# Optimization experiments

Hardware: AMD Instinct MI355X
Metric: run time of the kernel (lower is better)

The kernel has to match this reference:

```python
import jax, jax.numpy as jnp
import numpy as np

B, T, C, H = 8, 2048, 768, 64  # batch, block_size, n_embd, head_size

def setup_inputs() -> dict:
    key = jax.random.key(0)
    kx, kk, kq, kv = jax.random.split(key, 4)
    x = jax.random.normal(kx, (B, T, C), dtype=jnp.float32)
    Wk = jax.random.normal(kk, (C, H), dtype=jnp.float32) * (C ** -0.5)
    Wq = jax.random.normal(kq, (C, H), dtype=jnp.float32) * (C ** -0.5)
    Wv = jax.random.normal(kv, (C, H), dtype=jnp.float32) * (C ** -0.5)
    return {"x": x, "Wk": Wk, "Wq": Wq, "Wv": Wv}

def reference(x, Wk, Wq, Wv):
    # single causal self-attention head (dropout in eval mode = identity)
    k = jnp.einsum('btc,ch->bth', x, Wk)  # [B,T,H]
    q = jnp.einsum('btc,ch->bth', x, Wq)
    v = jnp.einsum('btc,ch->bth', x, Wv)
    scale = jnp.asarray(k.shape[-1], x.dtype) ** -0.5
    wei = jnp.einsum('bth,bsh->bts', q, k) * scale  # [B,T,T]
    t = x.shape[1]
    causal = jnp.tril(jnp.ones((t, t), dtype=bool))
    wei = jnp.where(causal[None, :, :], wei, jnp.asarray(-jnp.inf, wei.dtype))
    wei = jax.nn.softmax(wei, axis=-1)
    out = jnp.einsum('bts,bsh->bth', wei, v)  # [B,T,H]
    return out
```

## Files before the change

### kernel.cpp

```cpp
#include <hip/hip_runtime.h>
#include <hip/hip_bf16.h>

typedef __attribute__((ext_vector_type(8))) short short8;
typedef __attribute__((ext_vector_type(4))) float f32x4;

#define B_  8
#define T_  2048
#define C_  768
#define H_  64
#define M_  (B_ * T_)

static __device__ __forceinline__ unsigned short f2bf(float f) {
    __hip_bfloat16 h = __float2bfloat16(f);
    return *reinterpret_cast<unsigned short*>(&h);
}

static __device__ __forceinline__ short8 make_frag(const unsigned short* p0, const unsigned short* p1) {
    const ushort4 a = *reinterpret_cast<const ushort4*>(p0);
    const ushort4 b = *reinterpret_cast<const ushort4*>(p1);
    short8 r;
    r[0] = (short)a.x; r[1] = (short)a.y; r[2] = (short)a.z; r[3] = (short)a.w;
    r[4] = (short)b.x; r[5] = (short)b.y; r[6] = (short)b.z; r[7] = (short)b.w;
    return r;
}

static __device__ __forceinline__ int swz(int row, int u) {
    return row * 64 + ((((u) >> 3) ^ (row & 7)) << 3) + (u & 7);
}

static __device__ __forceinline__ int fragoff(int k) {
    const int half = k >> 5;
    const int kk   = k & 31;
    const int c    = half * 4 + ((kk >> 2) & 3);
    const int p    = (kk & 3) + ((kk & 16) >> 2);
    return c * 8 + p;
}

#define LOG2E_SCALE 0.18033688011112042f

__global__ __launch_bounds__(256) void prep_w(
    const float* __restrict__ Wq, const float* __restrict__ Wk, const float* __restrict__ Wv,
    unsigned short* __restrict__ Wt) {

    const int t   = threadIdx.x;
    const int mat = blockIdx.x / 48;
    const int kb  = blockIdx.x % 48;
    const int h   = t & 63;
    const int k0  = (kb * 4 + (t >> 6)) * 4;

    const float* Ws = (mat == 0) ? Wq : (mat == 1) ? Wk : Wv;
    const float sc  = (mat == 0) ? LOG2E_SCALE : 1.f;
    ushort4 o;
    o.x = f2bf(Ws[(size_t)(k0 + 0) * H_ + h] * sc);
    o.y = f2bf(Ws[(size_t)(k0 + 1) * H_ + h] * sc);
    o.z = f2bf(Ws[(size_t)(k0 + 2) * H_ + h] * sc);
    o.w = f2bf(Ws[(size_t)(k0 + 3) * H_ + h] * sc);
    *reinterpret_cast<ushort4*>(&Wt[(size_t)(mat * 64 + h) * C_ + k0]) = o;
}

__global__ __launch_bounds__(256) void proj_kernel(
    const float* __restrict__ x, const unsigned short* __restrict__ Wt,
    unsigned short* __restrict__ qkv) {

    __shared__ unsigned short Als[2][8192];

    const int tid = threadIdx.x;
    const int w   = tid >> 6;
    const int l   = tid & 63;
    const int lg  = l >> 4;
    const int lc  = l & 15;
    const int row0 = blockIdx.x * 64;

    const int sr   = tid >> 2;
    const int so   = tid & 3;
    const int srt  = sr >> 4;
    const int sr15 = sr & 15;
    const int sbase = (so * 16 + (sr15 ^ so)) * 8;

    f32x4 acc[4][3];
#pragma unroll
    for (int rt = 0; rt < 4; ++rt)
#pragma unroll
        for (int ct = 0; ct < 3; ++ct) acc[rt][ct] = (f32x4)0.f;

    const unsigned short* bbase[3];
#pragma unroll
    for (int ct = 0; ct < 3; ++ct)
        bbase[ct] = Wt + (size_t)(w * 48 + ct * 16 + lc) * C_ + lg * 8;

    const float* xrow = x + (size_t)(row0 + sr) * C_ + so * 8;

    float4 fa[4][2];
#pragma unroll
    for (int jj = 0; jj < 4; ++jj) {
        fa[jj][0] = *reinterpret_cast<const float4*>(xrow + jj * 32);
        fa[jj][1] = *reinterpret_cast<const float4*>(xrow + jj * 32 + 4);
    }

#pragma unroll
    for (int c = 0; c < 6; ++c) {
#pragma unroll
        for (int jj = 0; jj < 4; ++jj) {
            short8 v;
            v[0] = (short)f2bf(fa[jj][0].x); v[1] = (short)f2bf(fa[jj][0].y);
            v[2] = (short)f2bf(fa[jj][0].z); v[3] = (short)f2bf(fa[jj][0].w);
            v[4] = (short)f2bf(fa[jj][1].x); v[5] = (short)f2bf(fa[jj][1].y);
            v[6] = (short)f2bf(fa[jj][1].z); v[7] = (short)f2bf(fa[jj][1].w);
            *reinterpret_cast<short8*>(&Als[c & 1][(srt * 4 + jj) * 512 + sbase]) = v;
        }
        if (c < 5) {
#pragma unroll
            for (int jj = 0; jj < 4; ++jj) {
                fa[jj][0] = *reinterpret_cast<const float4*>(xrow + (c + 1) * 128 + jj * 32);
                fa[jj][1] = *reinterpret_cast<const float4*>(xrow + (c + 1) * 128 + jj * 32 + 4);
            }
        }
        __syncthreads();
#pragma unroll
        for (int kk = 0; kk < 4; ++kk) {
            short8 bcur[3];
#pragma unroll
            for (int ct = 0; ct < 3; ++ct)
                bcur[ct] = *reinterpret_cast<const short8*>(bbase[ct] + c * 128 + kk * 32);
            short8 af[4];
#pragma unroll
            for (int rt = 0; rt < 4; ++rt)
                af[rt] = *reinterpret_cast<const short8*>(
                    &Als[c & 1][(rt * 4 + kk) * 512 + (lg * 16 + (lc ^ lg)) * 8]);
#pragma unroll
            for (int rt = 0; rt < 4; ++rt)
#pragma unroll
                for (int ct = 0; ct < 3; ++ct)
                    acc[rt][ct] = __builtin_amdgcn_mfma_f32_16x16x32_bf16(af[rt], bcur[ct], acc[rt][ct], 0, 0, 0);
        }
    }

    __syncthreads();
    unsigned short* Ls = &Als[0][0];
#pragma unroll
    for (int ct = 0; ct < 3; ++ct) {
        const int col = w * 48 + ct * 16 + lc;
        const int mat = col >> 6;
        const int h   = col & 63;
        const int foh = fragoff(h);
#pragma unroll
        for (int rt = 0; rt < 4; ++rt)
#pragma unroll
            for (int j = 0; j < 4; ++j) {
                const int s6 = rt * 16 + lg * 4 + j;
                const unsigned short v = f2bf(acc[rt][ct][j]);
                if (mat == 0)      Ls[s6 * 64 + h] = v;
                else if (mat == 1) Ls[4096 + swz(s6, foh)] = v;
                else               Ls[8192 + swz(h, fragoff(s6))] = v;
            }
    }
    __syncthreads();

    unsigned short* Qd   = qkv;
    unsigned short* Kimg = qkv + (size_t)M_ * H_;
    unsigned short* Vimg = qkv + (size_t)2 * M_ * H_;
    const size_t g12 = (size_t)blockIdx.x << 12;
    const int o = tid * 8;
#pragma unroll
    for (int s = 0; s < 2; ++s) {
        const int off = s * 2048 + o;
        *reinterpret_cast<short8*>(&Qd[(size_t)row0 * 64 + off]) =
            *reinterpret_cast<const short8*>(&Ls[off]);
        *reinterpret_cast<short8*>(&Kimg[g12 + off]) =
            *reinterpret_cast<const short8*>(&Ls[4096 + off]);
        *reinterpret_cast<short8*>(&Vimg[g12 + off]) =
            *reinterpret_cast<const short8*>(&Ls[8192 + off]);
    }
}

#define SEG_FLOATS 4224

template<int SEG>
static __device__ __forceinline__ int segs_per_batch() { return SEG == 32 ? 32 : 80; }

template<int SEG>
static __device__ __forceinline__ void decode_seg(int r, int& qt, int& seg) {
    if (SEG == 32) { qt = r; seg = 0; return; }
    if (r < 8)       { qt = r;                seg = 0; }
    else if (r < 24) { qt = 8  + (r - 8) / 2; seg = (r - 8) & 1; }
    else if (r < 48) { qt = 16 + (r - 24) / 3; seg = (r - 24) % 3; }
    else             { qt = 24 + (r - 48) / 4; seg = (r - 48) & 3; }
}

template<int SEG>
static __device__ __forceinline__ int seg_prefix(int qt) {
    if (SEG == 32) return qt;
    if (qt < 8)  return qt;
    if (qt < 16) return 8  + 2 * (qt - 8);
    if (qt < 24) return 24 + 3 * (qt - 16);
    return 48 + 4 * (qt - 24);
}

template<int SEG>
__global__ __launch_bounds__(256) void attn_direct(
    const unsigned short* __restrict__ qkv, float* __restrict__ part,
    float* __restrict__ out) {

    const int spb = segs_per_batch<SEG>();
    const int b   = blockIdx.x / spb;
    const int rr  = spb - 1 - (blockIdx.x % spb);
    int qt, seg;
    decode_seg<SEG>(rr, qt, seg);

    const int tid = threadIdx.x;
    const int w  = tid >> 6;
    const int l  = tid & 63;
    const int lg = l >> 4;
    const int lc = l & 15;

    const unsigned short* Qg = qkv;
    const unsigned short* Kg = qkv + (size_t)M_ * H_;
    const unsigned short* Vg = qkv + (size_t)2 * M_ * H_;

    const unsigned short* qrow = Qg + (size_t)(b * T_ + qt * 64 + w * 16 + lc) * H_;
    short8 qf[2];
#pragma unroll
    for (int ks = 0; ks < 2; ++ks)
        qf[ks] = make_frag(qrow + ks * 32 + lg * 4, qrow + ks * 32 + lg * 4 + 16);

    int fo[2][4];
#pragma unroll
    for (int x = 0; x < 2; ++x)
#pragma unroll
        for (int y = 0; y < 4; ++y)
            fo[x][y] = swz(y * 16 + lc, (x * 4 + lg) * 8);

    float mval = -1e30f, lsum = 0.f;
    f32x4 oT[4];
#pragma unroll
    for (int t = 0; t < 4; ++t) oT[t] = (f32x4)0.f;

    const int q_glob = qt * 64 + w * 16 + lc;

    const int kv_beg = seg * SEG;
    const int kv_end = min(kv_beg + SEG, qt + 1);

    for (int kv = kv_beg; kv < kv_end; ++kv) {
        const size_t tb = ((size_t)(b * 32 + kv)) << 12;
        const unsigned short* Kt = Kg + tb;
        const unsigned short* Vt = Vg + tb;

        short8 kf[2][4];
#pragma unroll
        for (int ks = 0; ks < 2; ++ks)
#pragma unroll
            for (int st = 0; st < 4; ++st)
                kf[ks][st] = *reinterpret_cast<const short8*>(&Kt[fo[ks][st]]);

        f32x4 sT[4];
#pragma unroll
        for (int st = 0; st < 4; ++st) {
            f32x4 accs = (f32x4)0.f;
            accs = __builtin_amdgcn_mfma_f32_16x16x32_bf16(kf[0][st], qf[0], accs, 0, 0, 0);
            accs = __builtin_amdgcn_mfma_f32_16x16x32_bf16(kf[1][st], qf[1], accs, 0, 0, 0);
            sT[st] = accs;
        }

        short8 vf[2][4];
#pragma unroll
        for (int ks = 0; ks < 2; ++ks)
#pragma unroll
            for (int ht = 0; ht < 4; ++ht)
                vf[ks][ht] = *reinterpret_cast<const short8*>(&Vt[fo[ks][ht]]);

        float p[4][4];
#pragma unroll
        for (int st = 0; st < 4; ++st)
#pragma unroll
            for (int r = 0; r < 4; ++r)
                p[st][r] = sT[st][r];

        if (kv == qt) {
#pragma unroll
            for (int st = 0; st < 4; ++st)
#pragma unroll
                for (int r = 0; r < 4; ++r)
                    if ((kv * 64 + st * 16 + lg * 4 + r) > q_glob) p[st][r] = -1e30f;
        }

        float pm[4];
#pragma unroll
        for (int st = 0; st < 4; ++st)
            pm[st] = fmaxf(fmaxf(p[st][0], p[st][1]), fmaxf(p[st][2], p[st][3]));
        float pmax = fmaxf(fmaxf(pm[0], pm[1]), fmaxf(pm[2], pm[3]));
        pmax = fmaxf(pmax, __shfl_xor(pmax, 16));
        pmax = fmaxf(pmax, __shfl_xor(pmax, 32));

        if (!__all(pmax <= mval)) {
            const float mnew  = fmaxf(mval, pmax);
            const float alpha = exp2f(mval - mnew);
            mval = mnew;
            lsum *= alpha;
#pragma unroll
            for (int ht = 0; ht < 4; ++ht) oT[ht] *= alpha;
        }

        float ps[4];
#pragma unroll
        for (int st = 0; st < 4; ++st) {
#pragma unroll
            for (int r = 0; r < 4; ++r)
                p[st][r] = exp2f(p[st][r] - mval);
            ps[st] = (p[st][0] + p[st][1]) + (p[st][2] + p[st][3]);
        }
        float srow = (ps[0] + ps[1]) + (ps[2] + ps[3]);
        srow += __shfl_xor(srow, 16);
        srow += __shfl_xor(srow, 32);
        lsum += srow;

        short8 pb[2];
#pragma unroll
        for (int ks = 0; ks < 2; ++ks) {
#pragma unroll
            for (int r = 0; r < 4; ++r) {
                pb[ks][r]     = (short)f2bf(p[2 * ks][r]);
                pb[ks][r + 4] = (short)f2bf(p[2 * ks + 1][r]);
            }
        }

#pragma unroll
        for (int ks = 0; ks < 2; ++ks)
#pragma unroll
            for (int ht = 0; ht < 4; ++ht)
                oT[ht] = __builtin_amdgcn_mfma_f32_16x16x32_bf16(vf[ks][ht], pb[ks], oT[ht], 0, 0, 0);
    }

    const int nseg = (SEG == 32) ? 1 : (qt / 8 + 1);
    if (nseg == 1) {
        const float inv = 1.f / lsum;
        float* op = out + (size_t)(b * T_ + q_glob) * H_;
#pragma unroll
        for (int ht = 0; ht < 4; ++ht) {
            f32x4 v = oT[ht] * inv;
            *reinterpret_cast<f32x4*>(&op[ht * 16 + lg * 4]) = v;
        }
    } else {
        float* base = part + (size_t)(b * spb + seg_prefix<SEG>(qt) + seg) * SEG_FLOATS;
#pragma unroll
        for (int ht = 0; ht < 4; ++ht)
            *reinterpret_cast<f32x4*>(&base[(w * 16 + lc) * 64 + ht * 16 + lg * 4]) = oT[ht];
        if (lg == 0) {
            base[4096 + w * 16 + lc] = mval;
            base[4160 + w * 16 + lc] = lsum;
        }
    }
}

__global__ __launch_bounds__(256) void attn_merge8(
    const float* __restrict__ part, float* __restrict__ out) {

    const int b  = blockIdx.x / 24;
    const int qt = 8 + blockIdx.x % 24;
    const int nseg = qt / 8 + 1;
    const float* base0 = part + (size_t)(b * 80 + seg_prefix<8>(qt)) * SEG_FLOATS;

    const int tid = threadIdx.x;
    const int row = tid >> 2;
    const int c0  = (tid & 3) * 16;

    float M = -1e30f;
    for (int s = 0; s < nseg; ++s)
        M = fmaxf(M, base0[(size_t)s * SEG_FLOATS + 4096 + row]);

    float L = 0.f;
    f32x4 acc[4];
#pragma unroll
    for (int k = 0; k < 4; ++k) acc[k] = (f32x4)0.f;

    for (int s = 0; s < nseg; ++s) {
        const float* sb = base0 + (size_t)s * SEG_FLOATS;
        const float wsc = exp2f(sb[4096 + row] - M);
        L += sb[4160 + row] * wsc;
#pragma unroll
        for (int k = 0; k < 4; ++k) {
            const f32x4 ov = *reinterpret_cast<const f32x4*>(&sb[row * 64 + c0 + 4 * k]);
            acc[k] += ov * wsc;
        }
    }
    const float inv = 1.f / L;
    float* op = out + (size_t)(b * T_ + qt * 64 + row) * H_ + c0;
#pragma unroll
    for (int k = 0; k < 4; ++k)
        *reinterpret_cast<f32x4*>(&op[4 * k]) = acc[k] * inv;
}

extern "C" void kernel_launch(void* const* d_in, const int* in_sizes, int n_in,
                              void* d_out, int out_size, void* d_ws, size_t ws_size,
                              hipStream_t stream) {
    const float* x  = (const float*)d_in[0];
    const float* Wk = (const float*)d_in[1];
    const float* Wq = (const float*)d_in[2];
    const float* Wv = (const float*)d_in[3];

    const size_t qkvB = (size_t)3 * M_ * H_ * 2;
    const size_t WtB  = (size_t)3 * H_ * C_ * 2;
    unsigned short* qkv = (unsigned short*)d_ws;
    unsigned short* Wt  = (unsigned short*)((char*)d_ws + qkvB);
    float* part = (float*)((char*)d_ws + qkvB + WtB);
    float* out  = (float*)d_out;

    prep_w<<<dim3(144), dim3(256), 0, stream>>>(Wq, Wk, Wv, Wt);
    proj_kernel<<<dim3(M_ / 64), dim3(256), 0, stream>>>(x, Wt, qkv);

    const size_t need8 = qkvB + WtB + (size_t)(B_ * 80) * SEG_FLOATS * 4;
    if (ws_size >= need8) {
        attn_direct<8><<<dim3(B_ * 80), dim3(256), 0, stream>>>(qkv, part, out);
        attn_merge8<<<dim3(B_ * 24), dim3(256), 0, stream>>>(part, out);
    } else {
        attn_direct<32><<<dim3(B_ * 32), dim3(256), 0, stream>>>(qkv, part, out);
    }
}
```

Before: 58.14 us.

## Fuse weight prep, projection and attention into one cooperative kernel

Adds a cooperative-launch kernel that does weight conversion, QKV projection and causal attention in one launch, separated by grid-wide syncs, to remove inter-kernel launch gaps. In the fused path each block handles one full 64-row query tile with no kv splitting or merge, so work per block is unbalanced along the causal triangle. The old multi-kernel path is kept as a fallback, now always using the 8-tile split without checking the workspace size.

```diff
diff --git a/kernel.cpp b/kernel.cpp
--- a/kernel.cpp
+++ b/kernel.cpp
@@ -1,5 +1,8 @@
 #include <hip/hip_runtime.h>
 #include <hip/hip_bf16.h>
+#include <hip/hip_cooperative_groups.h>
+
+namespace cg = cooperative_groups;
 
 typedef __attribute__((ext_vector_type(8))) short short8;
 typedef __attribute__((ext_vector_type(4))) float f32x4;
@@ -37,6 +40,297 @@
 }
 
 #define LOG2E_SCALE 0.18033688011112042f
+
+
+static __device__ __forceinline__ void proj_body(
+    const float* __restrict__ x, const unsigned short* __restrict__ Wt,
+    unsigned short* __restrict__ qkv, unsigned short (*Als)[8192], int blk) {
+
+    const int tid = threadIdx.x;
+    const int w   = tid >> 6;
+    const int l   = tid & 63;
+    const int lg  = l >> 4;
+    const int lc  = l & 15;
+    const int row0 = blk * 64;
+
+    const int sr   = tid >> 2;
+    const int so   = tid & 3;
+    const int srt  = sr >> 4;
+    const int sr15 = sr & 15;
+    const int sbase = (so * 16 + (sr15 ^ so)) * 8;
+
+    f32x4 acc[4][3];
+#pragma unroll
+    for (int rt = 0; rt < 4; ++rt)
+#pragma unroll
+        for (int ct = 0; ct < 3; ++ct) acc[rt][ct] = (f32x4)0.f;
+
+    const unsigned short* bbase[3];
+#pragma unroll
+    for (int ct = 0; ct < 3; ++ct)
+        bbase[ct] = Wt + (size_t)(w * 48 + ct * 16 + lc) * C_ + lg * 8;
+
+    const float* xrow = x + (size_t)(row0 + sr) * C_ + so * 8;
+
+    float4 fa[4][2];
+#pragma unroll
+    for (int jj = 0; jj < 4; ++jj) {
+        fa[jj][0] = *reinterpret_cast<const float4*>(xrow + jj * 32);
+        fa[jj][1] = *reinterpret_cast<const float4*>(xrow + jj * 32 + 4);
+    }
+
+#pragma unroll
+    for (int c = 0; c < 6; ++c) {
+#pragma unroll
+        for (int jj = 0; jj < 4; ++jj) {
+            short8 v;
+            v[0] = (short)f2bf(fa[jj][0].x); v[1] = (short)f2bf(fa[jj][0].y);
+            v[2] = (short)f2bf(fa[jj][0].z); v[3] = (short)f2bf(fa[jj][0].w);
+            v[4] = (short)f2bf(fa[jj][1].x); v[5] = (short)f2bf(fa[jj][1].y);
+            v[6] = (short)f2bf(fa[jj][1].z); v[7] = (short)f2bf(fa[jj][1].w);
+            *reinterpret_cast<short8*>(&Als[c & 1][(srt * 4 + jj) * 512 + sbase]) = v;
+        }
+        if (c < 5) {
+#pragma unroll
+            for (int jj = 0; jj < 4; ++jj) {
+                fa[jj][0] = *reinterpret_cast<const float4*>(xrow + (c + 1) * 128 + jj * 32);
+                fa[jj][1] = *reinterpret_cast<const float4*>(xrow + (c + 1) * 128 + jj * 32 + 4);
+            }
+        }
+        __syncthreads();
+#pragma unroll
+        for (int kk = 0; kk < 4; ++kk) {
+            short8 bcur[3];
+#pragma unroll
+            for (int ct = 0; ct < 3; ++ct)
+                bcur[ct] = *reinterpret_cast<const short8*>(bbase[ct] + c * 128 + kk * 32);
+            short8 af[4];
+#pragma unroll
+            for (int rt = 0; rt < 4; ++rt)
+                af[rt] = *reinterpret_cast<const short8*>(
+                    &Als[c & 1][(rt * 4 + kk) * 512 + (lg * 16 + (lc ^ lg)) * 8]);
+#pragma unroll
+            for (int rt = 0; rt < 4; ++rt)
+#pragma unroll
+                for (int ct = 0; ct < 3; ++ct)
+                    acc[rt][ct] = __builtin_amdgcn_mfma_f32_16x16x32_bf16(af[rt], bcur[ct], acc[rt][ct], 0, 0, 0);
+        }
+    }
+
+    __syncthreads();
+    unsigned short* Ls = &Als[0][0];
+#pragma unroll
+    for (int ct = 0; ct < 3; ++ct) {
+        const int col = w * 48 + ct * 16 + lc;
+        const int mat = col >> 6;
+        const int h   = col & 63;
+        const int foh = fragoff(h);
+#pragma unroll
+        for (int rt = 0; rt < 4; ++rt)
+#pragma unroll
+            for (int j = 0; j < 4; ++j) {
+                const int s6 = rt * 16 + lg * 4 + j;
+                const unsigned short v = f2bf(acc[rt][ct][j]);
+                if (mat == 0)      Ls[s6 * 64 + h] = v;
+                else if (mat == 1) Ls[4096 + swz(s6, foh)] = v;
+                else               Ls[8192 + swz(h, fragoff(s6))] = v;
+            }
+    }
+    __syncthreads();
+
+    unsigned short* Qd   = qkv;
+    unsigned short* Kimg = qkv + (size_t)M_ * H_;
+    unsigned short* Vimg = qkv + (size_t)2 * M_ * H_;
+    const size_t g12 = (size_t)blk << 12;
+    const int o = tid * 8;
+#pragma unroll
+    for (int s = 0; s < 2; ++s) {
+        const int off = s * 2048 + o;
+        *reinterpret_cast<short8*>(&Qd[(size_t)row0 * 64 + off]) =
+            *reinterpret_cast<const short8*>(&Ls[off]);
+        *reinterpret_cast<short8*>(&Kimg[g12 + off]) =
+            *reinterpret_cast<const short8*>(&Ls[4096 + off]);
+        *reinterpret_cast<short8*>(&Vimg[g12 + off]) =
+            *reinterpret_cast<const short8*>(&Ls[8192 + off]);
+    }
+}
+
+static __device__ __forceinline__ void attn_body(
+    const unsigned short* __restrict__ qkv, int b, int qt,
+    int kv_beg, int kv_end, f32x4 oT[4], float& mval, float& lsum) {
+
+    const int tid = threadIdx.x;
+    const int w  = tid >> 6;
+    const int l  = tid & 63;
+    const int lg = l >> 4;
+    const int lc = l & 15;
+
+    const unsigned short* Qg = qkv;
+    const unsigned short* Kg = qkv + (size_t)M_ * H_;
+    const unsigned short* Vg = qkv + (size_t)2 * M_ * H_;
+
+    const unsigned short* qrow = Qg + (size_t)(b * T_ + qt * 64 + w * 16 + lc) * H_;
+    short8 qf[2];
+#pragma unroll
+    for (int ks = 0; ks < 2; ++ks)
+        qf[ks] = make_frag(qrow + ks * 32 + lg * 4, qrow + ks * 32 + lg * 4 + 16);
+
+    int fo[2][4];
+#pragma unroll
+    for (int xk = 0; xk < 2; ++xk)
+#pragma unroll
+        for (int y = 0; y < 4; ++y)
+            fo[xk][y] = swz(y * 16 + lc, (xk * 4 + lg) * 8);
+
+    const int q_glob = qt * 64 + w * 16 + lc;
+
+    for (int kv = kv_beg; kv < kv_end; ++kv) {
+        const size_t tb = ((size_t)(b * 32 + kv)) << 12;
+        const unsigned short* Kt = Kg + tb;
+        const unsigned short* Vt = Vg + tb;
+
+        short8 kf[2][4];
+#pragma unroll
+        for (int ks = 0; ks < 2; ++ks)
+#pragma unroll
+            for (int st = 0; st < 4; ++st)
+                kf[ks][st] = *reinterpret_cast<const short8*>(&Kt[fo[ks][st]]);
+
+        f32x4 sT[4];
+#pragma unroll
+        for (int st = 0; st < 4; ++st) {
+            f32x4 accs = (f32x4)0.f;
+            accs = __builtin_amdgcn_mfma_f32_16x16x32_bf16(kf[0][st], qf[0], accs, 0, 0, 0);
+            accs = __builtin_amdgcn_mfma_f32_16x16x32_bf16(kf[1][st], qf[1], accs, 0, 0, 0);
+            sT[st] = accs;
+        }
+
+        short8 vf[2][4];
+#pragma unroll
+        for (int ks = 0; ks < 2; ++ks)
+#pragma unroll
+            for (int ht = 0; ht < 4; ++ht)
+                vf[ks][ht] = *reinterpret_cast<const short8*>(&Vt[fo[ks][ht]]);
+
+        float p[4][4];
+#pragma unroll
+        for (int st = 0; st < 4; ++st)
+#pragma unroll
+            for (int r = 0; r < 4; ++r)
+                p[st][r] = sT[st][r];
+
+        if (kv == qt) {
+#pragma unroll
+            for (int st = 0; st < 4; ++st)
+#pragma unroll
+                for (int r = 0; r < 4; ++r)
+                    if ((kv * 64 + st * 16 + lg * 4 + r) > q_glob) p[st][r] = -1e30f;
+        }
+
+        float pm[4];
+#pragma unroll
+        for (int st = 0; st < 4; ++st)
+            pm[st] = fmaxf(fmaxf(p[st][0], p[st][1]), fmaxf(p[st][2], p[st][3]));
+        float pmax = fmaxf(fmaxf(pm[0], pm[1]), fmaxf(pm[2], pm[3]));
+        pmax = fmaxf(pmax, __shfl_xor(pmax, 16));
+        pmax = fmaxf(pmax, __shfl_xor(pmax, 32));
+
+        if (!__all(pmax <= mval)) {
+            const float mnew  = fmaxf(mval, pmax);
+            const float alpha = exp2f(mval - mnew);
+            mval = mnew;
+            lsum *= alpha;
+#pragma unroll
+            for (int ht = 0; ht < 4; ++ht) oT[ht] *= alpha;
+        }
+
+        float ps[4];
+#pragma unroll
+        for (int st = 0; st < 4; ++st) {
+#pragma unroll
+            for (int r = 0; r < 4; ++r)
+                p[st][r] = exp2f(p[st][r] - mval);
+            ps[st] = (p[st][0] + p[st][1]) + (p[st][2] + p[st][3]);
+        }
+        float srow = (ps[0] + ps[1]) + (ps[2] + ps[3]);
+        srow += __shfl_xor(srow, 16);
+        srow += __shfl_xor(srow, 32);
+        lsum += srow;
+
+        short8 pb[2];
+#pragma unroll
+        for (int ks = 0; ks < 2; ++ks) {
+#pragma unroll
+            for (int r = 0; r < 4; ++r) {
+                pb[ks][r]     = (short)f2bf(p[2 * ks][r]);
+                pb[ks][r + 4] = (short)f2bf(p[2 * ks + 1][r]);
+            }
+        }
+
+#pragma unroll
+        for (int ks = 0; ks < 2; ++ks)
+#pragma unroll
+            for (int ht = 0; ht < 4; ++ht)
+                oT[ht] = __builtin_amdgcn_mfma_f32_16x16x32_bf16(vf[ks][ht], pb[ks], oT[ht], 0, 0, 0);
+    }
+}
+
+__global__ __launch_bounds__(256) void fused_all(
+    const float* __restrict__ x,
+    const float* __restrict__ Wq, const float* __restrict__ Wk, const float* __restrict__ Wv,
+    unsigned short* __restrict__ Wt, unsigned short* __restrict__ qkv,
+    float* __restrict__ out) {
+
+    __shared__ unsigned short Als[2][8192];
+
+    {
+        const int g = blockIdx.x * 256 + threadIdx.x;
+        if (g < 36864) {
+            const int mat = g / 12288;
+            const int rem = g % 12288;
+            const int h   = rem & 63;
+            const int k0  = (rem >> 6) * 4;
+            const float* Ws = (mat == 0) ? Wq : (mat == 1) ? Wk : Wv;
+            const float sc  = (mat == 0) ? LOG2E_SCALE : 1.f;
+            ushort4 o;
+            o.x = f2bf(Ws[(size_t)(k0 + 0) * H_ + h] * sc);
+            o.y = f2bf(Ws[(size_t)(k0 + 1) * H_ + h] * sc);
+            o.z = f2bf(Ws[(size_t)(k0 + 2) * H_ + h] * sc);
+            o.w = f2bf(Ws[(size_t)(k0 + 3) * H_ + h] * sc);
+            *reinterpret_cast<ushort4*>(&Wt[(size_t)(mat * 64 + h) * C_ + k0]) = o;
+        }
+    }
+    cg::this_grid().sync();
+
+    proj_body(x, Wt, qkv, Als, blockIdx.x);
+
+    cg::this_grid().sync();
+
+    {
+        const int b  = blockIdx.x >> 5;
+        const int qt = 31 - (blockIdx.x & 31);
+
+        float mval = -1e30f, lsum = 0.f;
+        f32x4 oT[4];
+#pragma unroll
+        for (int t = 0; t < 4; ++t) oT[t] = (f32x4)0.f;
+
+        attn_body(qkv, b, qt, 0, qt + 1, oT, mval, lsum);
+
+        const int tid = threadIdx.x;
+        const int w  = tid >> 6;
+        const int l  = tid & 63;
+        const int lg = l >> 4;
+        const int lc = l & 15;
+        const float inv = 1.f / lsum;
+        float* op = out + (size_t)(b * T_ + qt * 64 + w * 16 + lc) * H_;
+#pragma unroll
+        for (int ht = 0; ht < 4; ++ht) {
+            f32x4 v = oT[ht] * inv;
+            *reinterpret_cast<f32x4*>(&op[ht * 16 + lg * 4]) = v;
+        }
+    }
+}
 
 __global__ __launch_bounds__(256) void prep_w(
     const float* __restrict__ Wq, const float* __restrict__ Wk, const float* __restrict__ Wv,
@@ -61,151 +355,43 @@
 __global__ __launch_bounds__(256) void proj_kernel(
     const float* __restrict__ x, const unsigned short* __restrict__ Wt,
     unsigned short* __restrict__ qkv) {
-
     __shared__ unsigned short Als[2][8192];
-
-    const int tid = threadIdx.x;
-    const int w   = tid >> 6;
-    const int l   = tid & 63;
-    const int lg  = l >> 4;
-    const int lc  = l & 15;
-    const int row0 = blockIdx.x * 64;
-
-    const int sr   = tid >> 2;
-    const int so   = tid & 3;
-    const int srt  = sr >> 4;
-    const int sr15 = sr & 15;
-    const int sbase = (so * 16 + (sr15 ^ so)) * 8;
-
-    f32x4 acc[4][3];
-#pragma unroll
-    for (int rt = 0; rt < 4; ++rt)
-#pragma unroll
-        for (int ct = 0; ct < 3; ++ct) acc[rt][ct] = (f32x4)0.f;
-
-    const unsigned short* bbase[3];
-#pragma unroll
-    for (int ct = 0; ct < 3; ++ct)
-        bbase[ct] = Wt + (size_t)(w * 48 + ct * 16 + lc) * C_ + lg * 8;
-
-    const float* xrow = x + (size_t)(row0 + sr) * C_ + so * 8;
-
-    float4 fa[4][2];
-#pragma unroll
-    for (int jj = 0; jj < 4; ++jj) {
-        fa[jj][0] = *reinterpret_cast<const float4*>(xrow + jj * 32);
-        fa[jj][1] = *reinterpret_cast<const float4*>(xrow + jj * 32 + 4);
-    }
-
-#pragma unroll
-    for (int c = 0; c < 6; ++c) {
-#pragma unroll
-        for (int jj = 0; jj < 4; ++jj) {
-            short8 v;
-            v[0] = (short)f2bf(fa[jj][0].x); v[1] = (short)f2bf(fa[jj][0].y);
-            v[2] = (short)f2bf(fa[jj][0].z); v[3] = (short)f2bf(fa[jj][0].w);
-            v[4] = (short)f2bf(fa[jj][1].x); v[5] = (short)f2bf(fa[jj][1].y);
-            v[6] = (short)f2bf(fa[jj][1].z); v[7] = (short)f2bf(fa[jj][1].w);
-            *reinterpret_cast<short8*>(&Als[c & 1][(srt * 4 + jj) * 512 + sbase]) = v;
-        }
-        if (c < 5) {
-#pragma unroll
-            for (int jj = 0; jj < 4; ++jj) {
-                fa[jj][0] = *reinterpret_cast<const float4*>(xrow + (c + 1) * 128 + jj * 32);
-                fa[jj][1] = *reinterpret_cast<const float4*>(xrow + (c + 1) * 128 + jj * 32 + 4);
-            }
-        }
-        __syncthreads();
-#pragma unroll
-        for (int kk = 0; kk < 4; ++kk) {
-            short8 bcur[3];
-#pragma unroll
-            for (int ct = 0; ct < 3; ++ct)
-                bcur[ct] = *reinterpret_cast<const short8*>(bbase[ct] + c * 128 + kk * 32);
-            short8 af[4];
-#pragma unroll
-            for (int rt = 0; rt < 4; ++rt)
-                af[rt] = *reinterpret_cast<const short8*>(
-                    &Als[c & 1][(rt * 4 + kk) * 512 + (lg * 16 + (lc ^ lg)) * 8]);
-#pragma unroll
-            for (int rt = 0; rt < 4; ++rt)
-#pragma unroll
-                for (int ct = 0; ct < 3; ++ct)
-                    acc[rt][ct] = __builtin_amdgcn_mfma_f32_16x16x32_bf16(af[rt], bcur[ct], acc[rt][ct], 0, 0, 0);
-        }
-    }
-
-    __syncthreads();
-    unsigned short* Ls = &Als[0][0];
-#pragma unroll
-    for (int ct = 0; ct < 3; ++ct) {
-        const int col = w * 48 + ct * 16 + lc;
-        const int mat = col >> 6;
-        const int h   = col & 63;
-        const int foh = fragoff(h);
-#pragma unroll
-        for (int rt = 0; rt < 4; ++rt)
-#pragma unroll
-            for (int j = 0; j < 4; ++j) {
-                const int s6 = rt * 16 + lg * 4 + j;
-                const unsigned short v = f2bf(acc[rt][ct][j]);
-                if (mat == 0)      Ls[s6 * 64 + h] = v;
-                else if (mat == 1) Ls[4096 + swz(s6, foh)] = v;
-                else               Ls[8192 + swz(h, fragoff(s6))] = v;
-            }
-    }
-    __syncthreads();
-
-    unsigned short* Qd   = qkv;
-    unsigned short* Kimg = qkv + (size_t)M_ * H_;
-    unsigned short* Vimg = qkv + (size_t)2 * M_ * H_;
-    const size_t g12 = (size_t)blockIdx.x << 12;
-    const int o = tid * 8;
-#pragma unroll
-    for (int s = 0; s < 2; ++s) {
-        const int off = s * 2048 + o;
-        *reinterpret_cast<short8*>(&Qd[(size_t)row0 * 64 + off]) =
-            *reinterpret_cast<const short8*>(&Ls[off]);
-        *reinterpret_cast<short8*>(&Kimg[g12 + off]) =
-            *reinterpret_cast<const short8*>(&Ls[4096 + off]);
-        *reinterpret_cast<short8*>(&Vimg[g12 + off]) =
-            *reinterpret_cast<const short8*>(&Ls[8192 + off]);
-    }
+    proj_body(x, Wt, qkv, Als, blockIdx.x);
 }
 
 #define SEG_FLOATS 4224
 
-template<int SEG>
-static __device__ __forceinline__ int segs_per_batch() { return SEG == 32 ? 32 : 80; }
-
-template<int SEG>
-static __device__ __forceinline__ void decode_seg(int r, int& qt, int& seg) {
-    if (SEG == 32) { qt = r; seg = 0; return; }
+static __device__ __forceinline__ void decode_seg8(int r, int& qt, int& seg) {
     if (r < 8)       { qt = r;                seg = 0; }
     else if (r < 24) { qt = 8  + (r - 8) / 2; seg = (r - 8) & 1; }
     else if (r < 48) { qt = 16 + (r - 24) / 3; seg = (r - 24) % 3; }
     else             { qt = 24 + (r - 48) / 4; seg = (r - 48) & 3; }
 }
 
-template<int SEG>
-static __device__ __forceinline__ int seg_prefix(int qt) {
-    if (SEG == 32) return qt;
+static __device__ __forceinline__ int seg_prefix8(int qt) {
     if (qt < 8)  return qt;
     if (qt < 16) return 8  + 2 * (qt - 8);
     if (qt < 24) return 24 + 3 * (qt - 16);
     return 48 + 4 * (qt - 24);
 }
 
-template<int SEG>
-__global__ __launch_bounds__(256) void attn_direct(
+__global__ __launch_bounds__(256) void attn_direct8(
     const unsigned short* __restrict__ qkv, float* __restrict__ part,
     float* __restrict__ out) {
 
-    const int spb = segs_per_batch<SEG>();
-    const int b   = blockIdx.x / spb;
-    const int rr  = spb - 1 - (blockIdx.x % spb);
+    const int b  = blockIdx.x / 80;
+    const int rr = 79 - (blockIdx.x % 80);
     int qt, seg;
-    decode_seg<SEG>(rr, qt, seg);
+    decode_seg8(rr, qt, seg);
+
+    float mval = -1e30f, lsum = 0.f;
+    f32x4 oT[4];
+#pragma unroll
+    for (int t = 0; t < 4; ++t) oT[t] = (f32x4)0.f;
+
+    const int kv_beg = seg * 8;
+    const int kv_end = min(kv_beg + 8, qt + 1);
+    attn_body(qkv, b, qt, kv_beg, kv_end, oT, mval, lsum);
 
     const int tid = threadIdx.x;
     const int w  = tid >> 6;
@@ -213,134 +399,17 @@
     const int lg = l >> 4;
     const int lc = l & 15;
 
-    const unsigned short* Qg = qkv;
-    const unsigned short* Kg = qkv + (size_t)M_ * H_;
-    const unsigned short* Vg = qkv + (size_t)2 * M_ * H_;
-
-    const unsigned short* qrow = Qg + (size_t)(b * T_ + qt * 64 + w * 16 + lc) * H_;
-    short8 qf[2];
-#pragma unroll
-    for (int ks = 0; ks < 2; ++ks)
-        qf[ks] = make_frag(qrow + ks * 32 + lg * 4, qrow + ks * 32 + lg * 4 + 16);
-
-    int fo[2][4];
-#pragma unroll
-    for (int x = 0; x < 2; ++x)
-#pragma unroll
-        for (int y = 0; y < 4; ++y)
-            fo[x][y] = swz(y * 16 + lc, (x * 4 + lg) * 8);
-
-    float mval = -1e30f, lsum = 0.f;
-    f32x4 oT[4];
-#pragma unroll
-    for (int t = 0; t < 4; ++t) oT[t] = (f32x4)0.f;
-
-    const int q_glob = qt * 64 + w * 16 + lc;
-
-    const int kv_beg = seg * SEG;
-    const int kv_end = min(kv_beg + SEG, qt + 1);
-
-    for (int kv = kv_beg; kv < kv_end; ++kv) {
-        const size_t tb = ((size_t)(b * 32 + kv)) << 12;
-        const unsigned short* Kt = Kg + tb;
-        const unsigned short* Vt = Vg + tb;
-
-        short8 kf[2][4];
-#pragma unroll
-        for (int ks = 0; ks < 2; ++ks)
-#pragma unroll
-            for (int st = 0; st < 4; ++st)
-                kf[ks][st] = *reinterpret_cast<const short8*>(&Kt[fo[ks][st]]);
-
-        f32x4 sT[4];
-#pragma unroll
-        for (int st = 0; st < 4; ++st) {
-            f32x4 accs = (f32x4)0.f;
-            accs = __builtin_amdgcn_mfma_f32_16x16x32_bf16(kf[0][st], qf[0], accs, 0, 0, 0);
-            accs = __builtin_amdgcn_mfma_f32_16x16x32_bf16(kf[1][st], qf[1], accs, 0, 0, 0);
-            sT[st] = accs;
-        }
-
-        short8 vf[2][4];
-#pragma unroll
-        for (int ks = 0; ks < 2; ++ks)
-#pragma unroll
-            for (int ht = 0; ht < 4; ++ht)
-                vf[ks][ht] = *reinterpret_cast<const short8*>(&Vt[fo[ks][ht]]);
-
-        float p[4][4];
-#pragma unroll
-        for (int st = 0; st < 4; ++st)
-#pragma unroll
-            for (int r = 0; r < 4; ++r)
-                p[st][r] = sT[st][r];
-
-        if (kv == qt) {
-#pragma unroll
-            for (int st = 0; st < 4; ++st)
-#pragma unroll
-                for (int r = 0; r < 4; ++r)
-                    if ((kv * 64 + st * 16 + lg * 4 + r) > q_glob) p[st][r] = -1e30f;
-        }
-
-        float pm[4];
-#pragma unroll
-        for (int st = 0; st < 4; ++st)
-            pm[st] = fmaxf(fmaxf(p[st][0], p[st][1]), fmaxf(p[st][2], p[st][3]));
-        float pmax = fmaxf(fmaxf(pm[0], pm[1]), fmaxf(pm[2], pm[3]));
-        pmax = fmaxf(pmax, __shfl_xor(pmax, 16));
-        pmax = fmaxf(pmax, __shfl_xor(pmax, 32));
-
-        if (!__all(pmax <= mval)) {
-            const float mnew  = fmaxf(mval, pmax);
-            const float alpha = exp2f(mval - mnew);
-            mval = mnew;
-            lsum *= alpha;
-#pragma unroll
-            for (int ht = 0; ht < 4; ++ht) oT[ht] *= alpha;
-        }
-
-        float ps[4];
-#pragma unroll
-        for (int st = 0; st < 4; ++st) {
-#pragma unroll
-            for (int r = 0; r < 4; ++r)
-                p[st][r] = exp2f(p[st][r] - mval);
-            ps[st] = (p[st][0] + p[st][1]) + (p[st][2] + p[st][3]);
-        }
-        float srow = (ps[0] + ps[1]) + (ps[2] + ps[3]);
-        srow += __shfl_xor(srow, 16);
-        srow += __shfl_xor(srow, 32);
-        lsum += srow;
-
-        short8 pb[2];
-#pragma unroll
-        for (int ks = 0; ks < 2; ++ks) {
-#pragma unroll
-            for (int r = 0; r < 4; ++r) {
-                pb[ks][r]     = (short)f2bf(p[2 * ks][r]);
-                pb[ks][r + 4] = (short)f2bf(p[2 * ks + 1][r]);
-            }
-        }
-
-#pragma unroll
-        for (int ks = 0; ks < 2; ++ks)
-#pragma unroll
-            for (int ht = 0; ht < 4; ++ht)
-                oT[ht] = __builtin_amdgcn_mfma_f32_16x16x32_bf16(vf[ks][ht], pb[ks], oT[ht], 0, 0, 0);
-    }
-
-    const int nseg = (SEG == 32) ? 1 : (qt / 8 + 1);
+    const int nseg = qt / 8 + 1;
     if (nseg == 1) {
         const float inv = 1.f / lsum;
-        float* op = out + (size_t)(b * T_ + q_glob) * H_;
+        float* op = out + (size_t)(b * T_ + qt * 64 + w * 16 + lc) * H_;
 #pragma unroll
         for (int ht = 0; ht < 4; ++ht) {
             f32x4 v = oT[ht] * inv;
             *reinterpret_cast<f32x4*>(&op[ht * 16 + lg * 4]) = v;
         }
     } else {
-        float* base = part + (size_t)(b * spb + seg_prefix<SEG>(qt) + seg) * SEG_FLOATS;
+        float* base = part + (size_t)(b * 80 + seg_prefix8(qt) + seg) * SEG_FLOATS;
 #pragma unroll
         for (int ht = 0; ht < 4; ++ht)
             *reinterpret_cast<f32x4*>(&base[(w * 16 + lc) * 64 + ht * 16 + lg * 4]) = oT[ht];
@@ -357,7 +426,7 @@
     const int b  = blockIdx.x / 24;
     const int qt = 8 + blockIdx.x % 24;
     const int nseg = qt / 8 + 1;
-    const float* base0 = part + (size_t)(b * 80 + seg_prefix<8>(qt)) * SEG_FLOATS;
+    const float* base0 = part + (size_t)(b * 80 + seg_prefix8(qt)) * SEG_FLOATS;
 
     const int tid = threadIdx.x;
     const int row = tid >> 2;
@@ -404,14 +473,19 @@
     float* part = (float*)((char*)d_ws + qkvB + WtB);
     float* out  = (float*)d_out;
 
+    {
+        const float* xa = x; const float* wqa = Wq; const float* wka = Wk; const float* wva = Wv;
+        unsigned short* wta = Wt; unsigned short* qa = qkv; float* oa = out;
+        void* args[] = { (void*)&xa, (void*)&wqa, (void*)&wka, (void*)&wva,
+                         (void*)&wta, (void*)&qa, (void*)&oa };
+        hipError_t e = hipLaunchCooperativeKernel((const void*)fused_all,
+                                                  dim3(256), dim3(256), args, 0, stream);
+        if (e == hipSuccess) return;
+        (void)hipGetLastError();
+    }
+
     prep_w<<<dim3(144), dim3(256), 0, stream>>>(Wq, Wk, Wv, Wt);
     proj_kernel<<<dim3(M_ / 64), dim3(256), 0, stream>>>(x, Wt, qkv);
-
-    const size_t need8 = qkvB + WtB + (size_t)(B_ * 80) * SEG_FLOATS * 4;
-    if (ws_size >= need8) {
-        attn_direct<8><<<dim3(B_ * 80), dim3(256), 0, stream>>>(qkv, part, out);
-        attn_merge8<<<dim3(B_ * 24), dim3(256), 0, stream>>>(part, out);
-    } else {
-        attn_direct<32><<<dim3(B_ * 32), dim3(256), 0, stream>>>(qkv, part, out);
-    }
-}
+    attn_direct8<<<dim3(B_ * 80), dim3(256), 0, stream>>>(qkv, part, out);
+    attn_merge8<<<dim3(B_ * 24), dim3(256), 0, stream>>>(part, out);
+}
```

After: 131.4 us. +126.0%, slower.
